# Performance work log

Hardware: AMD Instinct MI355X
Metric: run time of the kernel (lower is better)

## Reference

```python
import jax, jax.numpy as jnp
import numpy as np

B, L1, L2 = 8, 512, 512
FULL, HID, NLVL = 2048, 1024, 8
D = HID // NLVL  # attsize_per_lvl


def setup_inputs() -> dict:
    key = jax.random.key(0)
    k1, k2, k3, k4, k5, k6 = jax.random.split(key, 6)
    x1_att = jax.random.normal(k1, (B, L1, FULL), dtype=jnp.float32)
    x2_att = jax.random.normal(k2, (B, L2, FULL), dtype=jnp.float32)
    x2 = jax.random.normal(k3, (B, L2, HID), dtype=jnp.float32)
    x2_mask = jax.random.randint(k4, (B, L2), 0, 2).astype(bool)
    # nn.Linear(full_size, hidden_size, bias=False): weight [HID, FULL]
    W = jax.random.normal(k5, (HID, FULL), dtype=jnp.float32) / np.sqrt(FULL)
    final_v = jnp.ones((HID,), dtype=jnp.float32)  # linear_final param
    return {"x1_att": x1_att, "x2_att": x2_att, "x2": x2, "x2_mask": x2_mask,
            "W": W, "final_v": final_v}


def reference(x1_att, x2_att, x2, x2_mask, W, final_v):
    # dropout is identity in eval mode
    x1_key = jax.nn.relu(jnp.einsum('blf,hf->blh', x1_att, W))            # [B,L1,HID]
    x2_key = final_v * jax.nn.relu(jnp.einsum('blf,hf->blh', x2_att, W))  # [B,L2,HID]
    x1_rep = x1_key.reshape(B, L1, NLVL, D)  # split hidden into levels
    x2_rep = x2_key.reshape(B, L2, NLVL, D)
    scores = jnp.einsum('bqnd,bknd->bnqk', x1_rep, x2_rep)  # [B,NLVL,L1,L2]
    scores = jnp.where(x2_mask[:, None, None, :], -jnp.inf, scores)
    alpha = jax.nn.softmax(scores, axis=-1)                 # softmax over len2
    x2_lvl = x2.reshape(B, L2, NLVL, D)                     # value split per level
    atten = jnp.einsum('bnqk,bknd->bqnd', alpha, x2_lvl)    # [B,L1,NLVL,D]
    return atten.reshape(B, L1, HID)
```

## Files before the change

kernel.cpp:

```cpp
#include <hip/hip_runtime.h>
#include <stdint.h>

typedef _Float16 f16;
typedef _Float16 f16x8 __attribute__((ext_vector_type(8)));
typedef float f32x4 __attribute__((ext_vector_type(4)));
typedef float f32x16 __attribute__((ext_vector_type(16)));

typedef const __attribute__((address_space(1))) void* gas_ptr;
typedef __attribute__((address_space(3))) void* las_ptr;

__device__ __forceinline__ void gload16(const void* g, void* l) {
  __builtin_amdgcn_global_load_lds((gas_ptr)g, (las_ptr)l, 16, 0, 0);
}

#define OFF_A16 0u
#define OFF_W16 33554432u
#define OFF_K16 37748736u
#define OFF_VT  54525952u
#define WS_NEED 62914560u

__global__ void k_convert(const float* __restrict__ x1a, const float* __restrict__ x2a,
                          const float* __restrict__ W, f16* __restrict__ A16,
                          f16* __restrict__ W16) {
  const int NA = (8192 * 2048) / 8;
  const int NH = NA / 2;
  const int NW = (1024 * 2048) / 8;
  const int NT = NA + NW;
  for (int g = blockIdx.x * blockDim.x + threadIdx.x; g < NT; g += gridDim.x * blockDim.x) {
    const float* src;
    f16* dst;
    if (g < NA) {
      src = (g < NH) ? (x1a + 8 * (size_t)g) : (x2a + 8 * (size_t)(g - NH));
      dst = A16 + 8 * (size_t)g;
    } else {
      src = W + 8 * (size_t)(g - NA);
      dst = W16 + 8 * (size_t)(g - NA);
    }
    float4 v0 = *(const float4*)src;
    float4 v1 = *(const float4*)(src + 4);
    f16x8 h;
    h[0] = (f16)v0.x; h[1] = (f16)v0.y; h[2] = (f16)v0.z; h[3] = (f16)v0.w;
    h[4] = (f16)v1.x; h[5] = (f16)v1.y; h[6] = (f16)v1.z; h[7] = (f16)v1.w;
    *(f16x8*)dst = h;
  }
}

__global__ void k_transpose_v(const float* __restrict__ x2, f16* __restrict__ VT) {
  __shared__ f16 T[128 * 130];
  int bid = blockIdx.x;
  int kt = bid & 3, n = (bid >> 2) & 7, b = bid >> 5;
  int t = threadIdx.x;
  int k0 = kt * 128;
  #pragma unroll
  for (int p = 0; p < 16; ++p) {
    int kl = p * 8 + (t >> 5);
    int c4 = t & 31;
    float4 v = *(const float4*)(x2 + (size_t)(b * 512 + k0 + kl) * 1024 + n * 128 + c4 * 4);
    int d0 = c4 * 4;
    T[(d0 + 0) * 130 + kl] = (f16)v.x;
    T[(d0 + 1) * 130 + kl] = (f16)v.y;
    T[(d0 + 2) * 130 + kl] = (f16)v.z;
    T[(d0 + 3) * 130 + kl] = (f16)v.w;
  }
  __syncthreads();
  #pragma unroll
  for (int p = 0; p < 8; ++p) {
    int d = p * 16 + (t >> 4);
    int c = t & 15;
    f16x8 h;
    #pragma unroll
    for (int j = 0; j < 8; ++j) h[j] = T[d * 130 + c * 8 + j];
    *(f16x8*)(VT + (size_t)((b * 8 + n) * 128 + d) * 512 + k0 + c * 8) = h;
  }
}

__global__ void __launch_bounds__(256)
k_gemm_keys(const f16* __restrict__ A16, const f16* __restrict__ W16,
            const float* __restrict__ final_v, f16* __restrict__ K16) {
  __shared__ f16 Alds[64 * 128];
  __shared__ f16 Wlds[128 * 128];
  int bid = blockIdx.x;
  int sw = (bid & 7) * 128 + (bid >> 3);
  int mt = sw >> 3, nt = sw & 7;
  int t = threadIdx.x, l = t & 63, w = t >> 6;
  f32x16 acc[2];
  #pragma unroll
  for (int i = 0; i < 2; ++i)
    #pragma unroll
    for (int r = 0; r < 16; ++r) acc[i][r] = 0.f;
  bool isx2 = (mt >= 64);
  const char* Ab = (const char*)A16 + (size_t)mt * 64 * 4096;
  const char* Wb = (const char*)W16 + (size_t)nt * 128 * 4096;
  size_t soffA[4];
  #pragma unroll
  for (int i = 0; i < 4; ++i) {
    int row = (w * 4 + i) * 4 + (l >> 4);
    soffA[i] = (size_t)row * 4096 + (((l & 15) ^ (row & 15)) << 4);
  }
  size_t soffW[8];
  #pragma unroll
  for (int i = 0; i < 8; ++i) {
    int row = (w * 8 + i) * 4 + (l >> 4);
    soffW[i] = (size_t)row * 4096 + (((l & 15) ^ (row & 15)) << 4);
  }
  int g8 = l >> 5;
  int sxy = l & 15;
  const char* rdA0 = (const char*)Alds + (l & 31) * 256;
  const char* rdB0 = (const char*)Wlds + (w * 32 + (l & 31)) * 256;
  for (int ks = 0; ks < 16; ++ks) {
    int k0b = ks * 256;
    #pragma unroll
    for (int i = 0; i < 4; ++i)
      gload16(Ab + soffA[i] + k0b, (char*)Alds + (w * 4 + i) * 1024);
    #pragma unroll
    for (int i = 0; i < 8; ++i)
      gload16(Wb + soffW[i] + k0b, (char*)Wlds + (w * 8 + i) * 1024);
    __syncthreads();
    f16x8 af[2][8], bf[8];
    #pragma unroll
    for (int ks2 = 0; ks2 < 8; ++ks2) {
      int so = ((ks2 * 2 + g8) ^ sxy) << 4;
      af[0][ks2] = *(const f16x8*)(rdA0 + so);
      af[1][ks2] = *(const f16x8*)(rdA0 + 8192 + so);
      bf[ks2]    = *(const f16x8*)(rdB0 + so);
    }
    #pragma unroll
    for (int ks2 = 0; ks2 < 8; ++ks2) {
      acc[0] = __builtin_amdgcn_mfma_f32_32x32x16_f16(af[0][ks2], bf[ks2], acc[0], 0, 0, 0);
      acc[1] = __builtin_amdgcn_mfma_f32_32x32x16_f16(af[1][ks2], bf[ks2], acc[1], 0, 0, 0);
    }
    __syncthreads();
  }
  int c = l & 31, r2 = l >> 5;
  int col = nt * 128 + w * 32 + c;
  float fvv = isx2 ? final_v[col] : 1.0f;
  #pragma unroll
  for (int mi = 0; mi < 2; ++mi) {
    int rowbase = mt * 64 + mi * 32 + 4 * r2;
    #pragma unroll
    for (int r = 0; r < 16; ++r) {
      int row = rowbase + (r & 3) + 8 * (r >> 2);
      K16[(size_t)row * 1024 + col] = (f16)(fmaxf(acc[mi][r], 0.f) * fvv);
    }
  }
}

__global__ void __launch_bounds__(256)
k_attn(const f16* __restrict__ K16, const f16* __restrict__ VT,
       const int* __restrict__ mask, float* __restrict__ out) {
  __shared__ f16 Klds[2 * 64 * 128];
  __shared__ f16 Vlds[2 * 128 * 64];
  __shared__ f16 Plds[4 * 16 * 64];
  __shared__ float bias[512];
  int bid = blockIdx.x;
  int qt = bid & 7, n = (bid >> 3) & 7, b = bid >> 6;
  int t = threadIdx.x, l = t & 63, w = t >> 6;
  for (int i = t; i < 512; i += 256) bias[i] = mask[b * 512 + i] ? -1e30f : 0.0f;
  int r4 = l >> 4;
  int slot = (l & 15) << 4;
  int lg = r4 << 4;
  const char* Kg = (const char*)K16 + ((size_t)(4096 + b * 512) * 1024 + n * 128) * 2;
  const char* Vg = (const char*)VT + (size_t)((b * 8 + n) * 128) * 1024;
  int vr = l >> 3;
  int vslot = (l & 7) << 4;

#define STAGE_KV(ktv, bufsel) do {                                              \
    _Pragma("unroll")                                                           \
    for (int i_ = 0; i_ < 4; ++i_) {                                            \
      int rl_ = w * 16 + i_ * 4 + r4;                                           \
      gload16(Kg + (size_t)((ktv) * 64 + rl_) * 2048 + (slot ^ ((rl_ & 7) << 4)), \
              (char*)Klds + (bufsel) * 16384 + (w * 16 + i_ * 4) * 256);        \
    }                                                                           \
    _Pragma("unroll")                                                           \
    for (int i_ = 0; i_ < 4; ++i_) {                                            \
      int dl_ = w * 32 + i_ * 8 + vr;                                           \
      gload16(Vg + (size_t)dl_ * 1024 + (ktv) * 128 + (vslot ^ ((dl_ & 7) << 4)), \
              (char*)Vlds + (bufsel) * 16384 + (w * 32 + i_ * 8) * 128);        \
    }                                                                           \
  } while (0)

  const char* Qg = (const char*)K16 + ((size_t)(b * 512 + qt * 64) * 1024 + n * 128) * 2;
  int qrow = w * 16 + (l & 15);
  f16x8 qf[4];
  #pragma unroll
  for (int kk = 0; kk < 4; ++kk)
    qf[kk] = *(const f16x8*)(Qg + (size_t)qrow * 2048 + kk * 64 + lg);
  f32x4 o[8];
  #pragma unroll
  for (int dt = 0; dt < 8; ++dt) { o[dt][0] = 0.f; o[dt][1] = 0.f; o[dt][2] = 0.f; o[dt][3] = 0.f; }
  float m_r[4], l_r[4];
  #pragma unroll
  for (int r = 0; r < 4; ++r) { m_r[r] = -1e30f; l_r[r] = 0.0f; }
  char* Pw = (char*)Plds + w * 2048;

  STAGE_KV(0, 0);
  __syncthreads();
  #pragma unroll 8
  for (int kt = 0; kt < 8; ++kt) {
    int cur = kt & 1;
    if (kt < 7) STAGE_KV(kt + 1, cur ^ 1);
    const char* Kl = (const char*)Klds + cur * 16384;
    const char* Vl = (const char*)Vlds + cur * 16384;
    f32x4 s[4];
    #pragma unroll
    for (int nt4 = 0; nt4 < 4; ++nt4) {
      s[nt4][0] = 0.f; s[nt4][1] = 0.f; s[nt4][2] = 0.f; s[nt4][3] = 0.f;
      int krow = nt4 * 16 + (l & 15);
      int ksz = (krow & 7) << 4;
      #pragma unroll
      for (int kk = 0; kk < 4; ++kk) {
        f16x8 kf = *(const f16x8*)(Kl + krow * 256 + ((kk * 64 + lg) ^ ksz));
        s[nt4] = __builtin_amdgcn_mfma_f32_16x16x32_f16(qf[kk], kf, s[nt4], 0, 0, 0);
      }
      float bc = bias[kt * 64 + nt4 * 16 + (l & 15)];
      #pragma unroll
      for (int r = 0; r < 4; ++r) s[nt4][r] += bc;
    }
    float pmax[4], scale[4], csum[4];
    #pragma unroll
    for (int r = 0; r < 4; ++r)
      pmax[r] = fmaxf(fmaxf(s[0][r], s[1][r]), fmaxf(s[2][r], s[3][r]));
    #pragma unroll
    for (int off = 1; off <= 8; off <<= 1) {
      #pragma unroll
      for (int r = 0; r < 4; ++r) pmax[r] = fmaxf(pmax[r], __shfl_xor(pmax[r], off));
    }
    #pragma unroll
    for (int r = 0; r < 4; ++r) {
      float mn = fmaxf(m_r[r], pmax[r]);
      scale[r] = __expf(m_r[r] - mn);
      m_r[r] = mn;
      csum[r] = 0.0f;
    }
    #pragma unroll
    for (int nt4 = 0; nt4 < 4; ++nt4) {
      #pragma unroll
      for (int r = 0; r < 4; ++r) {
        float sv = s[nt4][r];
        float p = (sv <= -1e29f) ? 0.0f : __expf(sv - m_r[r]);
        csum[r] += p;
        int prow = (r4 << 2) + r;
        int addr = prow * 128 + (((nt4 * 16 + (l & 15)) * 2) ^ ((prow & 7) << 4));
        *(f16*)(Pw + addr) = (f16)p;
      }
    }
    #pragma unroll
    for (int off = 1; off <= 8; off <<= 1) {
      #pragma unroll
      for (int r = 0; r < 4; ++r) csum[r] += __shfl_xor(csum[r], off);
    }
    #pragma unroll
    for (int r = 0; r < 4; ++r) l_r[r] = l_r[r] * scale[r] + csum[r];
    #pragma unroll
    for (int dt = 0; dt < 8; ++dt) {
      #pragma unroll
      for (int r = 0; r < 4; ++r) o[dt][r] *= scale[r];
    }
    asm volatile("s_waitcnt lgkmcnt(0)" ::: "memory");
    int prow = l & 15;
    int psz = (prow & 7) << 4;
    f16x8 pf0 = *(const f16x8*)((const char*)Pw + prow * 128 + (lg ^ psz));
    f16x8 pf1 = *(const f16x8*)((const char*)Pw + prow * 128 + ((lg + 64) ^ psz));
    #pragma unroll
    for (int dt = 0; dt < 8; ++dt) {
      int drow = dt * 16 + (l & 15);
      int dsz = (drow & 7) << 4;
      f16x8 vf0 = *(const f16x8*)(Vl + drow * 128 + (lg ^ dsz));
      f16x8 vf1 = *(const f16x8*)(Vl + drow * 128 + ((lg + 64) ^ dsz));
      o[dt] = __builtin_amdgcn_mfma_f32_16x16x32_f16(pf0, vf0, o[dt], 0, 0, 0);
      o[dt] = __builtin_amdgcn_mfma_f32_16x16x32_f16(pf1, vf1, o[dt], 0, 0, 0);
    }
    __syncthreads();
  }
#undef STAGE_KV
  size_t ob = (size_t)(b * 512 + qt * 64 + w * 16 + (r4 << 2)) * 1024 + n * 128 + (l & 15);
  #pragma unroll
  for (int r = 0; r < 4; ++r) {
    float inv = 1.0f / fmaxf(l_r[r], 1e-30f);
    #pragma unroll
    for (int dt = 0; dt < 8; ++dt)
      out[ob + (size_t)r * 1024 + dt * 16] = o[dt][r] * inv;
  }
}

extern "C" void kernel_launch(void* const* d_in, const int* in_sizes, int n_in,
                              void* d_out, int out_size, void* d_ws, size_t ws_size,
                              hipStream_t stream) {
  const float* x1a = (const float*)d_in[0];
  const float* x2a = (const float*)d_in[1];
  const float* x2  = (const float*)d_in[2];
  const int*   msk = (const int*)d_in[3];
  const float* W   = (const float*)d_in[4];
  const float* fv  = (const float*)d_in[5];
  float* out = (float*)d_out;
  if (ws_size < (size_t)WS_NEED) return;
  char* ws = (char*)d_ws;
  f16* A16 = (f16*)(ws + OFF_A16);
  f16* W16 = (f16*)(ws + OFF_W16);
  f16* K16 = (f16*)(ws + OFF_K16);
  f16* VT  = (f16*)(ws + OFF_VT);
  k_convert<<<2048, 256, 0, stream>>>(x1a, x2a, W, A16, W16);
  k_transpose_v<<<256, 256, 0, stream>>>(x2, VT);
  k_gemm_keys<<<1024, 256, 0, stream>>>(A16, W16, fv, K16);
  k_attn<<<512, 256, 0, stream>>>(K16, VT, msk, out);
}
```

Before: 106.5 us.

## Merge prep kernels and enlarge key GEMM tile to 256x128 with 8 waves

```diff
diff --git a/kernel.cpp b/kernel.cpp
--- a/kernel.cpp
+++ b/kernel.cpp
@@ -19,14 +19,44 @@
 #define OFF_VT  54525952u
 #define WS_NEED 62914560u
 
-__global__ void k_convert(const float* __restrict__ x1a, const float* __restrict__ x2a,
-                          const float* __restrict__ W, f16* __restrict__ A16,
-                          f16* __restrict__ W16) {
+__global__ void k_prep(const float* __restrict__ x1a, const float* __restrict__ x2a,
+                       const float* __restrict__ x2, const float* __restrict__ W,
+                       f16* __restrict__ A16, f16* __restrict__ W16, f16* __restrict__ VT) {
+  __shared__ f16 T[128 * 130];
+  int t = threadIdx.x;
+  if (blockIdx.x < 256) {
+    int bid = blockIdx.x;
+    int kt = bid & 3, n = (bid >> 2) & 7, b = bid >> 5;
+    int k0 = kt * 128;
+    #pragma unroll
+    for (int p = 0; p < 16; ++p) {
+      int kl = p * 8 + (t >> 5);
+      int c4 = t & 31;
+      float4 v = *(const float4*)(x2 + (size_t)(b * 512 + k0 + kl) * 1024 + n * 128 + c4 * 4);
+      int d0 = c4 * 4;
+      T[(d0 + 0) * 130 + kl] = (f16)v.x;
+      T[(d0 + 1) * 130 + kl] = (f16)v.y;
+      T[(d0 + 2) * 130 + kl] = (f16)v.z;
+      T[(d0 + 3) * 130 + kl] = (f16)v.w;
+    }
+    __syncthreads();
+    #pragma unroll
+    for (int p = 0; p < 8; ++p) {
+      int d = p * 16 + (t >> 4);
+      int c = t & 15;
+      f16x8 h;
+      #pragma unroll
+      for (int j = 0; j < 8; ++j) h[j] = T[d * 130 + c * 8 + j];
+      *(f16x8*)(VT + (size_t)((b * 8 + n) * 128 + d) * 512 + k0 + c * 8) = h;
+    }
+    return;
+  }
   const int NA = (8192 * 2048) / 8;
   const int NH = NA / 2;
   const int NW = (1024 * 2048) / 8;
   const int NT = NA + NW;
-  for (int g = blockIdx.x * blockDim.x + threadIdx.x; g < NT; g += gridDim.x * blockDim.x) {
+  int stride = (gridDim.x - 256) * blockDim.x;
+  for (int g = (blockIdx.x - 256) * blockDim.x + t; g < NT; g += stride) {
     const float* src;
     f16* dst;
     if (g < NA) {
@@ -45,98 +75,72 @@
   }
 }
 
-__global__ void k_transpose_v(const float* __restrict__ x2, f16* __restrict__ VT) {
-  __shared__ f16 T[128 * 130];
-  int bid = blockIdx.x;
-  int kt = bid & 3, n = (bid >> 2) & 7, b = bid >> 5;
-  int t = threadIdx.x;
-  int k0 = kt * 128;
-  #pragma unroll
-  for (int p = 0; p < 16; ++p) {
-    int kl = p * 8 + (t >> 5);
-    int c4 = t & 31;
-    float4 v = *(const float4*)(x2 + (size_t)(b * 512 + k0 + kl) * 1024 + n * 128 + c4 * 4);
-    int d0 = c4 * 4;
-    T[(d0 + 0) * 130 + kl] = (f16)v.x;
-    T[(d0 + 1) * 130 + kl] = (f16)v.y;
-    T[(d0 + 2) * 130 + kl] = (f16)v.z;
-    T[(d0 + 3) * 130 + kl] = (f16)v.w;
-  }
-  __syncthreads();
-  #pragma unroll
-  for (int p = 0; p < 8; ++p) {
-    int d = p * 16 + (t >> 4);
-    int c = t & 15;
-    f16x8 h;
-    #pragma unroll
-    for (int j = 0; j < 8; ++j) h[j] = T[d * 130 + c * 8 + j];
-    *(f16x8*)(VT + (size_t)((b * 8 + n) * 128 + d) * 512 + k0 + c * 8) = h;
-  }
-}
-
-__global__ void __launch_bounds__(256)
+__global__ void __launch_bounds__(512)
 k_gemm_keys(const f16* __restrict__ A16, const f16* __restrict__ W16,
             const float* __restrict__ final_v, f16* __restrict__ K16) {
-  __shared__ f16 Alds[64 * 128];
+  __shared__ f16 Alds[256 * 128];
   __shared__ f16 Wlds[128 * 128];
   int bid = blockIdx.x;
-  int sw = (bid & 7) * 128 + (bid >> 3);
+  int sw = (bid & 7) * 32 + (bid >> 3);
   int mt = sw >> 3, nt = sw & 7;
   int t = threadIdx.x, l = t & 63, w = t >> 6;
-  f32x16 acc[2];
-  #pragma unroll
-  for (int i = 0; i < 2; ++i)
+  int wm = w >> 2, wn = w & 3;
+  f32x16 acc[4];
+  #pragma unroll
+  for (int i = 0; i < 4; ++i)
     #pragma unroll
     for (int r = 0; r < 16; ++r) acc[i][r] = 0.f;
-  bool isx2 = (mt >= 64);
-  const char* Ab = (const char*)A16 + (size_t)mt * 64 * 4096;
+  const char* Ab = (const char*)A16 + (size_t)mt * 256 * 4096;
   const char* Wb = (const char*)W16 + (size_t)nt * 128 * 4096;
-  size_t soffA[4];
+  size_t soffA[8];
+  #pragma unroll
+  for (int i = 0; i < 8; ++i) {
+    int u = i * 512 + w * 64 + l;
+    int row = u >> 4;
+    soffA[i] = (size_t)row * 4096 + (((l & 15) ^ (row & 15)) << 4);
+  }
+  size_t soffW[4];
   #pragma unroll
   for (int i = 0; i < 4; ++i) {
-    int row = (w * 4 + i) * 4 + (l >> 4);
-    soffA[i] = (size_t)row * 4096 + (((l & 15) ^ (row & 15)) << 4);
-  }
-  size_t soffW[8];
-  #pragma unroll
-  for (int i = 0; i < 8; ++i) {
-    int row = (w * 8 + i) * 4 + (l >> 4);
+    int u = i * 512 + w * 64 + l;
+    int row = u >> 4;
     soffW[i] = (size_t)row * 4096 + (((l & 15) ^ (row & 15)) << 4);
   }
   int g8 = l >> 5;
   int sxy = l & 15;
-  const char* rdA0 = (const char*)Alds + (l & 31) * 256;
-  const char* rdB0 = (const char*)Wlds + (w * 32 + (l & 31)) * 256;
+  const char* rdA0 = (const char*)Alds + (wm * 128 + (l & 31)) * 256;
+  const char* rdB0 = (const char*)Wlds + (wn * 32 + (l & 31)) * 256;
   for (int ks = 0; ks < 16; ++ks) {
     int k0b = ks * 256;
     #pragma unroll
+    for (int i = 0; i < 8; ++i)
+      gload16(Ab + soffA[i] + k0b, (char*)Alds + i * 8192 + w * 1024);
+    #pragma unroll
     for (int i = 0; i < 4; ++i)
-      gload16(Ab + soffA[i] + k0b, (char*)Alds + (w * 4 + i) * 1024);
-    #pragma unroll
-    for (int i = 0; i < 8; ++i)
-      gload16(Wb + soffW[i] + k0b, (char*)Wlds + (w * 8 + i) * 1024);
+      gload16(Wb + soffW[i] + k0b, (char*)Wlds + i * 8192 + w * 1024);
     __syncthreads();
-    f16x8 af[2][8], bf[8];
     #pragma unroll
     for (int ks2 = 0; ks2 < 8; ++ks2) {
       int so = ((ks2 * 2 + g8) ^ sxy) << 4;
-      af[0][ks2] = *(const f16x8*)(rdA0 + so);
-      af[1][ks2] = *(const f16x8*)(rdA0 + 8192 + so);
-      bf[ks2]    = *(const f16x8*)(rdB0 + so);
-    }
-    #pragma unroll
-    for (int ks2 = 0; ks2 < 8; ++ks2) {
-      acc[0] = __builtin_amdgcn_mfma_f32_32x32x16_f16(af[0][ks2], bf[ks2], acc[0], 0, 0, 0);
-      acc[1] = __builtin_amdgcn_mfma_f32_32x32x16_f16(af[1][ks2], bf[ks2], acc[1], 0, 0, 0);
+      f16x8 bf = *(const f16x8*)(rdB0 + so);
+      f16x8 a0 = *(const f16x8*)(rdA0 + so);
+      f16x8 a1 = *(const f16x8*)(rdA0 + 8192 + so);
+      f16x8 a2 = *(const f16x8*)(rdA0 + 16384 + so);
+      f16x8 a3 = *(const f16x8*)(rdA0 + 24576 + so);
+      acc[0] = __builtin_amdgcn_mfma_f32_32x32x16_f16(a0, bf, acc[0], 0, 0, 0);
+      acc[1] = __builtin_amdgcn_mfma_f32_32x32x16_f16(a1, bf, acc[1], 0, 0, 0);
+      acc[2] = __builtin_amdgcn_mfma_f32_32x32x16_f16(a2, bf, acc[2], 0, 0, 0);
+      acc[3] = __builtin_amdgcn_mfma_f32_32x32x16_f16(a3, bf, acc[3], 0, 0, 0);
     }
     __syncthreads();
   }
+  bool isx2 = (mt >= 16);
   int c = l & 31, r2 = l >> 5;
-  int col = nt * 128 + w * 32 + c;
+  int col = nt * 128 + wn * 32 + c;
   float fvv = isx2 ? final_v[col] : 1.0f;
   #pragma unroll
-  for (int mi = 0; mi < 2; ++mi) {
-    int rowbase = mt * 64 + mi * 32 + 4 * r2;
+  for (int mi = 0; mi < 4; ++mi) {
+    int rowbase = mt * 256 + wm * 128 + mi * 32 + 4 * r2;
     #pragma unroll
     for (int r = 0; r < 16; ++r) {
       int row = rowbase + (r & 3) + 8 * (r >> 2);
@@ -299,8 +303,7 @@
   f16* W16 = (f16*)(ws + OFF_W16);
   f16* K16 = (f16*)(ws + OFF_K16);
   f16* VT  = (f16*)(ws + OFF_VT);
-  k_convert<<<2048, 256, 0, stream>>>(x1a, x2a, W, A16, W16);
-  k_transpose_v<<<256, 256, 0, stream>>>(x2, VT);
-  k_gemm_keys<<<1024, 256, 0, stream>>>(A16, W16, fv, K16);
+  k_prep<<<2304, 256, 0, stream>>>(x1a, x2a, x2, W, A16, W16, VT);
+  k_gemm_keys<<<256, 512, 0, stream>>>(A16, W16, fv, K16);
   k_attn<<<512, 256, 0, stream>>>(K16, VT, msk, out);
 }
```

Result: faster. 97.78 us (-8.2%).
